# Performance work log

Measured on AMD Instinct MI355X. Metric: run time of the kernel, lower is better.

Reference implementation:

```python
import jax, jax.numpy as jnp
import numpy as np

EPS = 2e-5
N_ROT = 4  # p4 group: rotations by multiples of 90 degrees (exact via rot90)


def _conv2d(x, w, pad):
    # x: [B, Cin, H, W], w: [Cout, Cin, k, k]
    return jax.lax.conv_general_dilated(
        x, w, window_strides=(1, 1), padding=[(pad, pad), (pad, pad)],
        dimension_numbers=('NCHW', 'OIHW', 'NCHW'))


def _conv_rng(x, w):
    # Lifting (Rn -> G) conv. x: [B, I, H, W], w: [O, I, k, k] -> [B, O, 4, H', W']
    O, I, k, _ = w.shape
    wr = jnp.stack([jnp.rot90(w, r, axes=(-2, -1)) for r in range(N_ROT)])  # [4,O,I,k,k]
    y = _conv2d(x, wr.reshape(N_ROT * O, I, k, k), 0)  # [B, 4*O, H', W']
    B, _, H2, W2 = y.shape
    return y.reshape(B, N_ROT, O, H2, W2).transpose(0, 2, 1, 3, 4)


def _conv_gg(x, w, pad=0):
    # Group (G -> G) conv. x: [B, I, 4, H, W], w: [O, I, 4, k, k] -> [B, O, 4, H', W']
    O, I, _, k, _ = w.shape
    ws = []
    for r in range(N_ROT):
        wr = jnp.rot90(w, r, axes=(-2, -1))      # spatial rotation of the kernel
        wr = jnp.roll(wr, r, axis=2)              # cyclic shift of orientation axis
        ws.append(wr.reshape(O, I * N_ROT, k, k))
    wall = jnp.concatenate(ws, 0)                 # [4*O, I*4, k, k]
    B = x.shape[0]
    y = _conv2d(x.reshape(B, I * N_ROT, x.shape[-2], x.shape[-1]), wall, pad)
    H2, W2 = y.shape[-2:]
    return y.reshape(B, N_ROT, O, H2, W2).transpose(0, 2, 1, 3, 4)


def _att_rng(x, aw):
    # fSpatialAttention on Rn input: channel avg+max pooling -> 7x7 conv -> sigmoid gate.
    # x: [B, C, H, W], aw: [1, 2, 7, 7]
    pooled = jnp.concatenate([x.mean(1, keepdims=True), x.max(1, keepdims=True)], axis=1)
    att = jax.nn.sigmoid(_conv2d(pooled, aw, 3))  # [B,1,H,W], SAME padding
    return x * att


def _att_gg(x, aw):
    # fSpatialAttentionGG on G input: channel avg+max pooling -> equivariant 7x7 GG conv -> sigmoid.
    # x: [B, C, 4, H, W], aw: [1, 2, 4, 7, 7]
    pooled = jnp.concatenate([x.mean(1, keepdims=True), x.max(1, keepdims=True)], axis=1)
    att = jax.nn.sigmoid(_conv_gg(pooled, aw, pad=3))  # [B,1,4,H,W]
    return x * att


def _bn(x, g, b):
    # BatchNorm3d over [B, C, 4, H, W]: per-channel stats over (B, 4, H, W)
    m = x.mean((0, 2, 3, 4), keepdims=True)
    v = x.var((0, 2, 3, 4), keepdims=True)
    return (x - m) * jax.lax.rsqrt(v + EPS) * g.reshape(1, -1, 1, 1, 1) + b.reshape(1, -1, 1, 1, 1)


def _pool(x):
    # max_pooling_Rn: 2x2/2 spatial max pool applied independently per orientation
    return jax.lax.reduce_window(x, -jnp.inf, jax.lax.max,
                                 (1, 1, 1, 2, 2), (1, 1, 1, 2, 2), 'VALID')


def setup_inputs() -> dict:
    key = jax.random.key(0)
    ks = jax.random.split(key, 40)
    B, C = 2048, 10
    d = {'x': jax.random.normal(ks[0], (B, 1, 28, 28), jnp.float32)}
    d['c1_w'] = 0.2 * jax.random.normal(ks[1], (C, 1, 3, 3), jnp.float32)
    d['a1_w'] = 0.1 * jax.random.normal(ks[2], (1, 2, 7, 7), jnp.float32)
    j = 3
    for i in range(2, 7):
        d['c%d_w' % i] = 0.1 * jax.random.normal(ks[j], (C, C, 4, 3, 3), jnp.float32); j += 1
        d['a%d_w' % i] = 0.1 * jax.random.normal(ks[j], (1, 2, 4, 7, 7), jnp.float32); j += 1
    d['c7_w'] = 0.1 * jax.random.normal(ks[j], (10, C, 4, 4, 4), jnp.float32); j += 1
    d['a7_w'] = 0.1 * jax.random.normal(ks[j], (1, 2, 4, 7, 7), jnp.float32); j += 1
    for i in range(1, 7):
        d['bn%d_g' % i] = jnp.ones((C,), jnp.float32)
        d['bn%d_b' % i] = jnp.zeros((C,), jnp.float32)
    return d


def reference(x, c1_w, a1_w, c2_w, a2_w, c3_w, a3_w, c4_w, a4_w, c5_w, a5_w,
              c6_w, a6_w, c7_w, a7_w, bn1_g, bn1_b, bn2_g, bn2_b, bn3_g, bn3_b,
              bn4_g, bn4_b, bn5_g, bn5_b, bn6_g, bn6_b):
    # Dropout is treated as identity (eval mode / deterministic reference).
    out = jax.nn.relu(_bn(_conv_rng(_att_rng(x, a1_w), c1_w), bn1_g, bn1_b))      # [B,10,4,26,26]
    out = jax.nn.relu(_bn(_conv_gg(_att_gg(out, a2_w), c2_w), bn2_g, bn2_b))       # [B,10,4,24,24]
    out = _pool(out)                                                                # [B,10,4,12,12]
    out = jax.nn.relu(_bn(_conv_gg(_att_gg(out, a3_w), c3_w), bn3_g, bn3_b))       # 10x10
    out = jax.nn.relu(_bn(_conv_gg(_att_gg(out, a4_w), c4_w), bn4_g, bn4_b))       # 8x8
    out = jax.nn.relu(_bn(_conv_gg(_att_gg(out, a5_w), c5_w), bn5_g, bn5_b))       # 6x6
    out = jax.nn.relu(_bn(_conv_gg(_att_gg(out, a6_w), c6_w), bn6_g, bn6_b))       # 4x4
    out = _conv_gg(_att_gg(out, a7_w), c7_w)                                        # [B,10,4,1,1]
    out = out.max(axis=2)                                                           # group max-pool over orientations
    return out.reshape(out.shape[0], 10)
```

## Files before the change

kernel.cpp:

```cpp
#include <hip/hip_runtime.h>
#include <hip/hip_bf16.h>
#include <cstddef>

typedef __hip_bfloat16 bf;
typedef __attribute__((ext_vector_type(8))) short short8x;
typedef __attribute__((ext_vector_type(4))) float f32x4;

__device__ __forceinline__ float ldv(const float* p){ return *p; }
__device__ __forceinline__ float ldv(const bf* p){ return __bfloat162float(*p); }
__device__ __forceinline__ void stv(float* p, float v){ *p = v; }
__device__ __forceinline__ void stv(bf* p, float v){ *p = __float2bfloat16(v); }
__device__ __forceinline__ float sigm(float x){ return 1.f/(1.f + __expf(-x)); }
__device__ __forceinline__ short bfbits(float v){
  __hip_bfloat16 h = __float2bfloat16(v);
  return *(short*)&h;
}

__device__ __forceinline__ float ldin(const void* p, long i, int f32){
  return f32 ? ((const float*)p)[i] : __bfloat162float(((const bf*)p)[i]);
}

template<int K>
__device__ __forceinline__ int rot_src(int r, int t){
  int u = t / K, v = t % K;
  int s1 = v*K + (K-1-u);
  int s2 = (K-1-u)*K + (K-1-v);
  int s3 = (K-1-v)*K + u;
  return r==0 ? t : (r==1 ? s1 : (r==2 ? s2 : s3));
}

__global__ void k_detect(const void* x, int* ctrl){
  int lane = threadIdx.x;
  float mx = 0.f;
  for (int i = lane; i < 2048; i += 64){
    float v = __bfloat162float(((const bf*)x)[i]);
    if (v != v) v = 1e30f;
    mx = fmaxf(mx, fabsf(v));
  }
  #pragma unroll
  for (int off = 32; off > 0; off >>= 1) mx = fmaxf(mx, __shfl_xor(mx, off));
  if (lane == 0) ctrl[0] = (mx > 1e6f) ? 1 : 0;
}

__global__ __launch_bounds__(256) void k_build_bt(const void* c2, const void* c3, const void* c4,
                                                  const int* __restrict__ ctrl, short* __restrict__ btg){
  const void* ws[3] = {c2, c3, c4};
  const void* cw = ws[blockIdx.x];
  short* outp = btg + blockIdx.x * 18432;
  int f32 = ctrl[0];
  for (int i = threadIdx.x; i < 18432; i += 256){
    int t, n, k;
    bool valid;
    if (i < 13824){
      t = i / 1536;
      int rem = i % 1536;
      int kq = rem / 384;
      n = (i >> 3) % 48;
      k = kq*8 + (i & 7);
      valid = (n < 40);
    } else {
      int j2 = i - 13824;
      int tg = j2 / 1536;
      int lq = (j2 % 1536) / 384;
      n = (j2 >> 3) % 48;
      k = 32 + (i & 7);
      t = tg*4 + lq;
      valid = (t < 9) && (n < 40);
    }
    float v = 0.f;
    if (valid){
      int o = n >> 2, r = n & 3, ci = k >> 2, s = k & 3;
      v = ldin(cw, ((o*10 + ci)*4 + ((s - r) & 3))*9 + rot_src<3>(r, t), f32);
    }
    outp[i] = bfbits(v);
  }
}

__global__ __launch_bounds__(256) void k_l1(const void* __restrict__ x,
                                            const void* __restrict__ a1,
                                            const void* __restrict__ c1,
                                            const int* __restrict__ ctrl,
                                            float* __restrict__ xa,
                                            float* __restrict__ ssum, float* __restrict__ ssq){
  __shared__ float xs[784];
  __shared__ float ws[49];
  __shared__ float xg[28*29];
  __shared__ float wr1[360];
  __shared__ float lsum[16], lss[16];
  int b = blockIdx.x, tid = threadIdx.x;
  int f32 = ctrl[0];
  for (int i = tid; i < 784; i += 256) xs[i] = ldin(x, (long)b*784 + i, f32);
  if (tid < 49) ws[tid] = ldin(a1, tid, f32) + ldin(a1, 49 + tid, f32);
  for (int i = tid; i < 360; i += 256){
    int r = i / 90, rem = i % 90, o = rem / 9, t = rem % 9;
    wr1[i] = ldin(c1, o*9 + rot_src<3>(r, t), f32);
  }
  if (tid < 16){ lsum[tid] = 0.f; lss[tid] = 0.f; }
  __syncthreads();
  for (int p = tid; p < 784; p += 256){
    int h = p / 28, w = p % 28;
    float acc = 0.f;
    #pragma unroll
    for (int u = 0; u < 7; ++u){
      int hh = h + u - 3;
      if (hh < 0 || hh >= 28) continue;
      #pragma unroll
      for (int v = 0; v < 7; ++v){
        int ww = w + v - 3;
        if (ww < 0 || ww >= 28) continue;
        acc = fmaf(xs[hh*28 + ww], ws[u*7 + v], acc);
      }
    }
    float g = xs[p] * sigm(acc);
    xg[h*29 + w] = g;
    xa[(size_t)b*784 + p] = g;
  }
  __syncthreads();
  for (int it = tid; it < 1040; it += 256){
    int o = it / 104, rem = it % 104, r = rem / 26, h = rem % 26;
    float wt[9];
    #pragma unroll
    for (int t = 0; t < 9; ++t) wt[t] = wr1[(r*10 + o)*9 + t];
    float acc[26];
    #pragma unroll
    for (int w = 0; w < 26; ++w) acc[w] = 0.f;
    #pragma unroll
    for (int u = 0; u < 3; ++u){
      float rr[28];
      #pragma unroll
      for (int j = 0; j < 28; ++j) rr[j] = xg[(h + u)*29 + j];
      #pragma unroll
      for (int v = 0; v < 3; ++v){
        float wv = wt[u*3 + v];
        #pragma unroll
        for (int w = 0; w < 26; ++w) acc[w] = fmaf(rr[w + v], wv, acc[w]);
      }
    }
    float s1 = 0.f, s2 = 0.f;
    #pragma unroll
    for (int w = 0; w < 26; ++w){ s1 += acc[w]; s2 += acc[w]*acc[w]; }
    atomicAdd(&lsum[o], s1); atomicAdd(&lss[o], s2);
  }
  __syncthreads();
  if (tid < 10){ atomicAdd(&ssum[tid], lsum[tid]); atomicAdd(&ssq[tid], lss[tid]); }
}

__global__ void k_finalize(const float* __restrict__ ssum, const float* __restrict__ ssq,
                           const void* __restrict__ g, const void* __restrict__ bb,
                           const int* __restrict__ ctrl,
                           float invN, float* __restrict__ scale, float* __restrict__ shift){
  int c = threadIdx.x;
  if (c < 10){
    float m = ssum[c] * invN;
    float v = fmaxf(ssq[c] * invN - m*m, 0.f);
    float sc = ldin(g, c, ctrl[0]) * rsqrtf(v + 2e-5f);
    scale[c] = sc;
    shift[c] = ldin(bb, c, ctrl[0]) - m * sc;
  }
}

__global__ __launch_bounds__(128) void k_att2(const float* __restrict__ xa,
                                              const void* __restrict__ c1,
                                              const float* __restrict__ sc1,
                                              const float* __restrict__ sh1,
                                              const void* __restrict__ aw,
                                              const int* __restrict__ ctrl,
                                              float* __restrict__ attf){
  __shared__ float xs[28*29];
  __shared__ float wr1[360];
  __shared__ float ps[8*26*33];
  __shared__ float wl[1568];
  __shared__ float scs[10], shs[10];
  int b = blockIdx.x, tid = threadIdx.x;
  int f32 = ctrl[0];
  for (int i = tid; i < 784; i += 128){
    int row = i / 28, col = i % 28;
    xs[row*29 + col] = xa[(size_t)b*784 + i];
  }
  for (int i = tid; i < 360; i += 128){
    int r = i / 90, rem = i % 90, o = rem / 9, t = rem % 9;
    wr1[i] = ldin(c1, o*9 + rot_src<3>(r, t), f32);
  }
  for (int i = tid; i < 8*26*33; i += 128) ps[i] = 0.f;
  for (int i = tid; i < 1568; i += 128){
    int r = i / 392, rem = i % 392, i2 = rem / 196, s = (rem % 196)/49, t = rem % 49;
    int sp = (s - r) & 3;
    wl[i] = ldin(aw, (i2*4 + sp)*49 + rot_src<7>(r, t), f32);
  }
  if (tid < 10){ scs[tid] = sc1[tid]; shs[tid] = sh1[tid]; }
  __syncthreads();
  if (tid < 104){
    int s = tid / 26, h = tid % 26;
    float msum[26], mmax[26];
    #pragma unroll
    for (int w = 0; w < 26; ++w){ msum[w] = 0.f; mmax[w] = 0.f; }
    for (int o = 0; o < 10; ++o){
      const float* wb = wr1 + (s*10 + o)*9;
      float acc[26];
      #pragma unroll
      for (int w = 0; w < 26; ++w) acc[w] = 0.f;
      #pragma unroll
      for (int u = 0; u < 3; ++u){
        float rr[28];
        #pragma unroll
        for (int j = 0; j < 28; ++j) rr[j] = xs[(h + u)*29 + j];
        #pragma unroll
        for (int v = 0; v < 3; ++v){
          float wv = wb[u*3 + v];
          #pragma unroll
          for (int w = 0; w < 26; ++w) acc[w] = fmaf(rr[w + v], wv, acc[w]);
        }
      }
      float a_sc = scs[o], a_sh = shs[o];
      #pragma unroll
      for (int w = 0; w < 26; ++w){
        float val = fmaxf(fmaf(acc[w], a_sc, a_sh), 0.f);
        msum[w] += val; mmax[w] = fmaxf(mmax[w], val);
      }
    }
    #pragma unroll
    for (int w = 0; w < 26; ++w){
      ps[s*858 + h*33 + 3 + w] = msum[w] * 0.1f;
      ps[(4 + s)*858 + h*33 + 3 + w] = mmax[w];
    }
  }
  __syncthreads();
  if (tid < 104){
    int r = tid / 26, h = tid % 26;
    float acc[26];
    #pragma unroll
    for (int w = 0; w < 26; ++w) acc[w] = 0.f;
    for (int c = 0; c < 8; ++c){
      const float* wb = wl + r*392 + c*49;
      const float* pb = ps + c*858;
      #pragma unroll
      for (int u = 0; u < 7; ++u){
        int row = h + u - 3;
        if (row < 0 || row >= 26) continue;
        float rr[32];
        #pragma unroll
        for (int j = 0; j < 32; ++j) rr[j] = pb[row*33 + j];
        #pragma unroll
        for (int v = 0; v < 7; ++v){
          float wv = wb[u*7 + v];
          #pragma unroll
          for (int w = 0; w < 26; ++w) acc[w] = fmaf(rr[w + v], wv, acc[w]);
        }
      }
    }
    size_t base = ((size_t)b*4 + r)*676 + (size_t)h*26;
    #pragma unroll
    for (int w = 0; w < 26; ++w) attf[base + w] = sigm(acc[w]);
  }
}

__global__ __launch_bounds__(512, 4) void k_conv2m(const float* __restrict__ xa,
                                                const void* __restrict__ c1,
                                                const float* __restrict__ sc1,
                                                const float* __restrict__ sh1,
                                                const float* __restrict__ attm,
                                                const short* __restrict__ btg,
                                                const int* __restrict__ ctrl,
                                                bf* __restrict__ ap2,
                                                float* __restrict__ ssum, float* __restrict__ ssq){
  __shared__ alignas(16) float xs2[784];
  __shared__ float wr1[360];
  __shared__ alignas(16) float attL[4*676];
  __shared__ alignas(16) short xin[676*40];
  __shared__ float lsum[16], lss[16];
  int tid = threadIdx.x, b = blockIdx.x;
  int f32 = ctrl[0];
  for (int i = tid; i < 784; i += 512) xs2[i] = xa[(size_t)b*784 + i];
  for (int i = tid; i < 360; i += 512){
    int r = i / 90, rem = i % 90, o = rem / 9, t = rem % 9;
    wr1[i] = ldin(c1, o*9 + rot_src<3>(r, t), f32);
  }
  for (int i = tid; i < 2704; i += 512) attL[i] = attm[(size_t)b*2704 + i];
  if (tid < 16){ lsum[tid] = 0.f; lss[tid] = 0.f; }
  __syncthreads();
  for (int it = tid; it < 1040; it += 512){
    int row = it / 40, ch = it % 40;
    int ci = ch >> 2, s = ch & 3;
    float wt[9];
    {
      const float* wb = wr1 + (s*10 + ci)*9;
      #pragma unroll
      for (int t = 0; t < 9; ++t) wt[t] = wb[t];
    }
    float sc = sc1[ci], sh = sh1[ci];
    float acc[26];
    #pragma unroll
    for (int w = 0; w < 26; ++w) acc[w] = 0.f;
    #pragma unroll
    for (int u = 0; u < 3; ++u){
      float rr[28];
      const float4* rp = (const float4*)(xs2 + (row + u)*28);
      #pragma unroll
      for (int j = 0; j < 7; ++j){ float4 q = rp[j]; rr[4*j]=q.x; rr[4*j+1]=q.y; rr[4*j+2]=q.z; rr[4*j+3]=q.w; }
      #pragma unroll
      for (int v = 0; v < 3; ++v){
        float wv = wt[u*3 + v];
        #pragma unroll
        for (int w = 0; w < 26; ++w) acc[w] = fmaf(rr[w + v], wv, acc[w]);
      }
    }
    const float* ap = attL + s*676 + row*26;
    #pragma unroll
    for (int w = 0; w < 26; ++w){
      float v = fmaxf(fmaf(acc[w], sc, sh), 0.f) * ap[w];
      xin[(row*26 + w)*40 + ch] = bfbits(v);
    }
  }
  __syncthreads();

  int wv = tid >> 6, lane = tid & 63, lm = lane & 15, lq = lane >> 4;
  short8x bmain[9], btail[3];
  int tdh[3], tdw[3];
  #pragma unroll
  for (int tg = 0; tg < 3; ++tg){
    int tap = tg*4 + lq; if (tap > 8) tap = 8;
    tdh[tg] = tap / 3; tdw[tg] = tap % 3;
  }
  int curNt = -1, n = 0, o = 0;
  for (int u = wv; u < 54; u += 8){
    int nt = u / 18, mp = u % 18;
    if (nt != curNt){
      curNt = nt; n = nt*16 + lm; o = n >> 2;
      #pragma unroll
      for (int t = 0; t < 9; ++t)
        bmain[t] = *(const short8x*)(btg + (((t*4 + lq)*48 + n) << 3));
      #pragma unroll
      for (int tg = 0; tg < 3; ++tg)
        btail[tg] = *(const short8x*)(btg + 13824 + (((tg*4 + lq)*48 + n) << 3));
    }
    int mt0 = mp*2, mt1 = mp*2 + 1;
    int mA0 = mt0*16 + lm, mA1 = mt1*16 + lm;
    int qi0 = mA0 >> 2, sub0 = mA0 & 3;
    int h00 = 2*(qi0/12) + (sub0 >> 1), w00 = 2*(qi0%12) + (sub0 & 1);
    int qi1 = mA1 >> 2, sub1 = mA1 & 3;
    int h01 = 2*(qi1/12) + (sub1 >> 1), w01 = 2*(qi1%12) + (sub1 & 1);
    f32x4 acc0 = {0.f,0.f,0.f,0.f}, acc1 = {0.f,0.f,0.f,0.f};
    #pragma unroll
    for (int t = 0; t < 9; ++t){
      int sp0 = (h00 + t/3)*26 + (w00 + t%3);
      int sp1 = (h01 + t/3)*26 + (w01 + t%3);
      short8x a0 = *(const short8x*)&xin[sp0*40 + lq*8];
      short8x a1 = *(const short8x*)&xin[sp1*40 + lq*8];
      acc0 = __builtin_amdgcn_mfma_f32_16x16x32_bf16(a0, bmain[t], acc0, 0, 0, 0);
      acc1 = __builtin_amdgcn_mfma_f32_16x16x32_bf16(a1, bmain[t], acc1, 0, 0, 0);
    }
    #pragma unroll
    for (int tg = 0; tg < 3; ++tg){
      int sp0 = (h00 + tdh[tg])*26 + (w00 + tdw[tg]);
      int sp1 = (h01 + tdh[tg])*26 + (w01 + tdw[tg]);
      short8x a0 = *(const short8x*)&xin[sp0*40 + 32];
      short8x a1 = *(const short8x*)&xin[sp1*40 + 32];
      acc0 = __builtin_amdgcn_mfma_f32_16x16x32_bf16(a0, btail[tg], acc0, 0, 0, 0);
      acc1 = __builtin_amdgcn_mfma_f32_16x16x32_bf16(a1, btail[tg], acc1, 0, 0, 0);
    }
    if (n < 40){
      float s1 = acc0[0]+acc0[1]+acc0[2]+acc0[3] + acc1[0]+acc1[1]+acc1[2]+acc1[3];
      float s2 = acc0[0]*acc0[0]+acc0[1]*acc0[1]+acc0[2]*acc0[2]+acc0[3]*acc0[3]
               + acc1[0]*acc1[0]+acc1[1]*acc1[1]+acc1[2]*acc1[2]+acc1[3]*acc1[3];
      atomicAdd(&lsum[o], s1); atomicAdd(&lss[o], s2);
      float mx0 = fmaxf(fmaxf(acc0[0], acc0[1]), fmaxf(acc0[2], acc0[3]));
      float mx1 = fmaxf(fmaxf(acc1[0], acc1[1]), fmaxf(acc1[2], acc1[3]));
      size_t pbase = ((size_t)b*40 + n)*144;
      stv(ap2 + pbase + mt0*4 + lq, mx0);
      stv(ap2 + pbase + mt1*4 + lq, mx1);
    }
  }
  __syncthreads();
  if (tid < 10){ atomicAdd(&ssum[tid], lsum[tid]); atomicAdd(&ssq[tid], lss[tid]); }
}

template<int HIN, int WIN, int NT, typename TI>
__global__ __launch_bounds__(NT) void k_conv_ggm(const TI* __restrict__ act,
                                                 const float* __restrict__ scale,
                                                 const float* __restrict__ shift,
                                                 const float* __restrict__ attm,
                                                 const short* __restrict__ btg,
                                                 float* __restrict__ out,
                                                 float* __restrict__ ssum, float* __restrict__ ssq){
  constexpr int HOUT = HIN - 2, WOUT = WIN - 2;
  constexpr int M = HOUT*WOUT, HW = HIN*WIN;
  constexpr int MT = (M + 15)/16, MU = (MT + 1)/2, UNITS = MU*3;
  constexpr int NWV = NT/64;
  __shared__ alignas(16) short xin[HW*40];
  __shared__ float lsum[16], lss[16];
  int tid = threadIdx.x, b = blockIdx.x;
  if (tid < 16){ lsum[tid] = 0.f; lss[tid] = 0.f; }
  for (int i = tid; i < HW*40; i += NT){
    int sp = i / 40, ch = i % 40;
    int ci = ch >> 2, s = ch & 3;
    float a = ldv(act + ((size_t)b*40 + ch)*HW + sp);
    a = fmaxf(fmaf(a, scale[ci], shift[ci]), 0.f);
    xin[i] = bfbits(a * attm[((size_t)b*4 + s)*HW + sp]);
  }
  __syncthreads();
  int wv = tid >> 6, lane = tid & 63, lm = lane & 15, lq = lane >> 4;
  short8x bmain[9], btail[3];
  int tdh[3], tdw[3];
  #pragma unroll
  for (int tg = 0; tg < 3; ++tg){
    int tap = tg*4 + lq; if (tap > 8) tap = 8;
    tdh[tg] = tap / 3; tdw[tg] = tap % 3;
  }
  int curNt = -1, n = 0, o = 0;
  for (int u = wv; u < UNITS; u += NWV){
    int nt = u / MU, mu = u % MU;
    if (nt != curNt){
      curNt = nt; n = nt*16 + lm; o = n >> 2;
      #pragma unroll
      for (int t = 0; t < 9; ++t)
        bmain[t] = *(const short8x*)(btg + (((t*4 + lq)*48 + n) << 3));
      #pragma unroll
      for (int tg = 0; tg < 3; ++tg)
        btail[tg] = *(const short8x*)(btg + 13824 + (((tg*4 + lq)*48 + n) << 3));
    }
    int mt0 = mu*2, mt1 = mu*2 + 1;
    int mA0 = mt0*16 + lm; if (mA0 > M-1) mA0 = M-1;
    int mA1 = mt1*16 + lm; if (mA1 > M-1) mA1 = M-1;
    int mh0 = mA0 / WOUT, mw0 = mA0 % WOUT;
    int mh1 = mA1 / WOUT, mw1 = mA1 % WOUT;
    f32x4 acc0 = {0.f,0.f,0.f,0.f}, acc1 = {0.f,0.f,0.f,0.f};
    #pragma unroll
    for (int t = 0; t < 9; ++t){
      int sp0 = (mh0 + t/3)*WIN + (mw0 + t%3);
      int sp1 = (mh1 + t/3)*WIN + (mw1 + t%3);
      short8x a0 = *(const short8x*)&xin[sp0*40 + lq*8];
      short8x a1 = *(const short8x*)&xin[sp1*40 + lq*8];
      acc0 = __builtin_amdgcn_mfma_f32_16x16x32_bf16(a0, bmain[t], acc0, 0, 0, 0);
      acc1 = __builtin_amdgcn_mfma_f32_16x16x32_bf16(a1, bmain[t], acc1, 0, 0, 0);
    }
    #pragma unroll
    for (int tg = 0; tg < 3; ++tg){
      int sp0 = (mh0 + tdh[tg])*WIN + (mw0 + tdw[tg]);
      int sp1 = (mh1 + tdh[tg])*WIN + (mw1 + tdw[tg]);
      short8x a0 = *(const short8x*)&xin[sp0*40 + 32];
      short8x a1 = *(const short8x*)&xin[sp1*40 + 32];
      acc0 = __builtin_amdgcn_mfma_f32_16x16x32_bf16(a0, btail[tg], acc0, 0, 0, 0);
      acc1 = __builtin_amdgcn_mfma_f32_16x16x32_bf16(a1, btail[tg], acc1, 0, 0, 0);
    }
    if (n < 40){
      float s1 = 0.f, s2 = 0.f;
      size_t obase = ((size_t)b*40 + n)*M;
      #pragma unroll
      for (int reg = 0; reg < 4; ++reg){
        int m0 = mt0*16 + lq*4 + reg;
        if (m0 < M){ float v = acc0[reg]; s1 += v; s2 += v*v; out[obase + m0] = v; }
        int m1 = mt1*16 + lq*4 + reg;
        if (m1 < M){ float v = acc1[reg]; s1 += v; s2 += v*v; out[obase + m1] = v; }
      }
      atomicAdd(&lsum[o], s1); atomicAdd(&lss[o], s2);
    }
  }
  __syncthreads();
  if (tid < 10){ atomicAdd(&ssum[tid], lsum[tid]); atomicAdd(&ssq[tid], lss[tid]); }
}

template<int H, int W, int NT, typename TA>
__global__ __launch_bounds__(NT) void k_att_gg(const TA* __restrict__ act,
                                               const float* __restrict__ scale,
                                               const float* __restrict__ shift,
                                               const void* __restrict__ aw,
                                               const int* __restrict__ ctrl,
                                               float* __restrict__ att){
  constexpr int WG = (W + 6) | 1;
  constexpr int HW = H*W;
  __shared__ float ps[8*H*WG];
  __shared__ float wl[1568];
  int b = blockIdx.x, tid = threadIdx.x;
  int f32 = ctrl[0];
  for (int i = tid; i < 4*H*WG; i += NT){
    int s = i / (H*WG), rem = i % (H*WG), row = rem / WG, col = rem % WG;
    int cc = col - 3;
    float mn = 0.f, mx = 0.f;
    if (cc >= 0 && cc < W){
      float sum = 0.f; mx = 0.f;
      const TA* ap = act + (size_t)b*40*HW + (size_t)s*HW + row*W + cc;
      #pragma unroll
      for (int c = 0; c < 10; ++c){
        float v = fmaxf(fmaf(ldv(ap + (size_t)c*4*HW), scale[c], shift[c]), 0.f);
        sum += v; mx = fmaxf(mx, v);
      }
      mn = sum * 0.1f;
    }
    ps[s*H*WG + row*WG + col] = mn;
    ps[(4 + s)*H*WG + row*WG + col] = mx;
  }
  for (int i = tid; i < 1568; i += NT){
    int r = i / 392, rem = i % 392, i2 = rem / 196, s = (rem % 196)/49, t = rem % 49;
    int sp = (s - r) & 3;
    wl[i] = ldin(aw, (i2*4 + sp)*49 + rot_src<7>(r, t), f32);
  }
  __syncthreads();
  for (int it = tid; it < 4*H; it += NT){
    int r = it / H, h = it % H;
    float acc[W];
    #pragma unroll
    for (int w = 0; w < W; ++w) acc[w] = 0.f;
    for (int c = 0; c < 8; ++c){
      const float* wb = wl + r*392 + c*49;
      const float* pb = ps + c*H*WG;
      #pragma unroll
      for (int u = 0; u < 7; ++u){
        int row = h + u - 3;
        if (row < 0 || row >= H) continue;
        float rr[W + 6];
        #pragma unroll
        for (int j = 0; j < W + 6; ++j) rr[j] = pb[row*WG + j];
        #pragma unroll
        for (int v = 0; v < 7; ++v){
          float wv = wb[u*7 + v];
          #pragma unroll
          for (int w = 0; w < W; ++w) acc[w] = fmaf(rr[w + v], wv, acc[w]);
        }
      }
    }
    size_t base = ((size_t)b*4 + r)*HW + (size_t)h*W;
    #pragma unroll
    for (int w = 0; w < W; ++w) att[base + w] = sigm(acc[w]);
  }
}

template<int HIN, int WIN, int K, int SR, int NT, bool STATS, typename TI, typename TO>
__global__ __launch_bounds__(NT) void k_conv_gg(const TI* __restrict__ act,
                                                const float* __restrict__ scale,
                                                const float* __restrict__ shift,
                                                const float* __restrict__ attm,
                                                const void* __restrict__ cw,
                                                const int* __restrict__ ctrl,
                                                TO* __restrict__ out,
                                                float* __restrict__ ssum, float* __restrict__ ssq){
  constexpr int HOUT = HIN - K + 1;
  constexpr int WOUT = WIN - K + 1;
  constexpr int NS   = HOUT / SR;
  constexpr int WP   = WIN | 1;
  constexpr int NW   = 10*10*4*K*K;
  __shared__ float xin[40*HIN*WP];
  __shared__ float wl[NW];
  __shared__ float lsum[16], lss[16];
  int tid = threadIdx.x;
  int b = blockIdx.x;
  int f32 = ctrl[0];
  for (int i = tid; i < 40*HIN*WP; i += NT){
    int c = i / (HIN*WP), rem = i % (HIN*WP), rr = rem / WP, col = rem % WP;
    float v = 0.f;
    if (col < WIN){
      int ch = c >> 2, s = c & 3;
      float a = ldv(act + ((size_t)b*40 + c)*HIN*WIN + (size_t)rr*WIN + col);
      a = fmaxf(fmaf(a, scale[ch], shift[ch]), 0.f);
      v = a * attm[((size_t)b*4 + s)*HIN*WIN + (size_t)rr*WIN + col];
    }
    xin[i] = v;
  }
  for (int i = tid; i < NW; i += NT) wl[i] = ldin(cw, i, f32);
  if (STATS && tid < 16){ lsum[tid] = 0.f; lss[tid] = 0.f; }
  __syncthreads();
  for (int it = tid; it < 40*NS; it += NT){
    int o = it / (4*NS), rem = it % (4*NS), r = rem / NS, hs = rem % NS;
    int h0 = hs * SR;
    int perm[K*K];
    #pragma unroll
    for (int t = 0; t < K*K; ++t) perm[t] = rot_src<K>(r, t);
    float acc[SR][WOUT];
    #pragma unroll
    for (int a = 0; a < SR; ++a)
      #pragma unroll
      for (int w = 0; w < WOUT; ++w) acc[a][w] = 0.f;
    for (int ci = 0; ci < 10; ++ci){
      #pragma unroll
      for (int s = 0; s < 4; ++s){
        int sp = (s - r) & 3;
        const float* wb = wl + (size_t)((o*10 + ci)*4 + sp)*K*K;
        float wt[K*K];
        #pragma unroll
        for (int t = 0; t < K*K; ++t) wt[t] = wb[perm[t]];
        const float* ib = xin + (ci*4 + s)*HIN*WP;
        #pragma unroll
        for (int ri = 0; ri < SR + K - 1; ++ri){
          float rr[WP];
          #pragma unroll
          for (int j = 0; j < WP; ++j) rr[j] = ib[(h0 + ri)*WP + j];
          #pragma unroll
          for (int u = 0; u < K; ++u){
            int orr = ri - u;
            if (orr < 0 || orr >= SR) continue;
            #pragma unroll
            for (int v = 0; v < K; ++v){
              float wv = wt[u*K + v];
              #pragma unroll
              for (int w = 0; w < WOUT; ++w) acc[orr][w] = fmaf(rr[w + v], wv, acc[orr][w]);
            }
          }
        }
      }
    }
    if (STATS){
      float s1 = 0.f, s2 = 0.f;
      #pragma unroll
      for (int a = 0; a < SR; ++a)
        #pragma unroll
        for (int w = 0; w < WOUT; ++w){ s1 += acc[a][w]; s2 += acc[a][w]*acc[a][w]; }
      atomicAdd(&lsum[o], s1); atomicAdd(&lss[o], s2);
    }
    #pragma unroll
    for (int a = 0; a < SR; ++a){
      size_t base = ((size_t)b*40 + o*4 + r)*HOUT*WOUT + (size_t)(h0 + a)*WOUT;
      #pragma unroll
      for (int w = 0; w < WOUT; ++w) stv(out + base + w, acc[a][w]);
    }
  }
  if (STATS){
    __syncthreads();
    if (tid < 10){ atomicAdd(&ssum[tid], lsum[tid]); atomicAdd(&ssq[tid], lss[tid]); }
  }
}

__global__ __launch_bounds__(256) void k_out_max(const float* __restrict__ y7, void* __restrict__ outp,
                                                 const int* __restrict__ ctrl){
  int idx = blockIdx.x * 256 + threadIdx.x;
  if (idx >= 20480) return;
  int f32 = ctrl[0];
  const float* p = y7 + (size_t)idx*4;
  float m = fmaxf(fmaxf(p[0], p[1]), fmaxf(p[2], p[3]));
  if (f32) ((float*)outp)[idx] = m;
  else stv((bf*)outp + idx, m);
}

extern "C" void kernel_launch(void* const* d_in, const int* in_sizes, int n_in,
                              void* d_out, int out_size, void* d_ws, size_t ws_size,
                              hipStream_t stream){
  (void)in_sizes; (void)n_in; (void)out_size; (void)ws_size;
  const void* x  = d_in[0];
  const void* c1 = d_in[1];
  const void* a1 = d_in[2];
  const void* c2 = d_in[3];
  const void* a2 = d_in[4];
  const void* c3 = d_in[5];
  const void* a3 = d_in[6];
  const void* c4 = d_in[7];
  const void* a4 = d_in[8];
  const void* c5 = d_in[9];
  const void* a5 = d_in[10];
  const void* c6 = d_in[11];
  const void* a6 = d_in[12];
  const void* c7 = d_in[13];
  const void* a7 = d_in[14];
  const void* bng[6] = {d_in[15],d_in[17],d_in[19],d_in[21],d_in[23],d_in[25]};
  const void* bnb[6] = {d_in[16],d_in[18],d_in[20],d_in[22],d_in[24],d_in[26]};

  size_t off = 0;
  char* wsb = (char*)d_ws;
  auto alloc = [&](size_t bytes)->void*{ void* p = wsb + off; off += (bytes + 255) & ~(size_t)255; return p; };
  int*   ctrl   = (int*)alloc(256);
  float* stats  = (float*)alloc(192*sizeof(float));
  float* scales = (float*)alloc(192*sizeof(float));
  short* btfr   = (short*)alloc(3*18432*2);
  char*  region1 = (char*)alloc(28573696);
  bf*    ap2 = (bf*)alloc((size_t)2048*40*144*2);
  float* yD  = (float*)alloc((size_t)2048*40*100*4);
  float* xa    = (float*)region1;
  float* attf2 = (float*)(region1 + 6422528);
  float* yE    = (float*)region1;
  float* attf3 = (float*)(region1 + 20971520);

  hipMemsetAsync(ctrl, 0, 1024, stream);
  k_detect<<<1, 64, 0, stream>>>(x, ctrl);
  k_build_bt<<<3, 256, 0, stream>>>(c2, c3, c4, ctrl, btfr);

  k_l1<<<2048, 256, 0, stream>>>(x, a1, c1, ctrl, xa, stats + 0, stats + 16);
  k_finalize<<<1, 64, 0, stream>>>(stats + 0, stats + 16, bng[0], bnb[0], ctrl, 1.f/5537792.f, scales + 0, scales + 16);

  k_att2<<<2048, 128, 0, stream>>>(xa, c1, scales + 0, scales + 16, a2, ctrl, attf2);
  k_conv2m<<<2048, 512, 0, stream>>>(xa, c1, scales + 0, scales + 16, attf2, btfr, ctrl, ap2, stats + 32, stats + 48);
  k_finalize<<<1, 64, 0, stream>>>(stats + 32, stats + 48, bng[1], bnb[1], ctrl, 1.f/4718592.f, scales + 32, scales + 48);

  k_att_gg<12,12,64,bf><<<2048, 64, 0, stream>>>(ap2, scales + 32, scales + 48, a3, ctrl, attf3);
  k_conv_ggm<12,12,256,bf><<<2048, 256, 0, stream>>>(ap2, scales + 32, scales + 48,
                                                     attf3, btfr + 18432, yD, stats + 64, stats + 80);
  k_finalize<<<1, 64, 0, stream>>>(stats + 64, stats + 80, bng[2], bnb[2], ctrl, 1.f/819200.f, scales + 64, scales + 80);

  k_att_gg<10,10,64,float><<<2048, 64, 0, stream>>>(yD, scales + 64, scales + 80, a4, ctrl, attf3);
  k_conv_ggm<10,10,128,float><<<2048, 128, 0, stream>>>(yD, scales + 64, scales + 80,
                                                        attf3, btfr + 36864, yE, stats + 96, stats + 112);
  k_finalize<<<1, 64, 0, stream>>>(stats + 96, stats + 112, bng[3], bnb[3], ctrl, 1.f/524288.f, scales + 96, scales + 112);

  k_att_gg<8,8,64,float><<<2048, 64, 0, stream>>>(yE, scales + 96, scales + 112, a5, ctrl, attf3);
  k_conv_gg<8,8,3,2,192,true,float,float><<<2048, 192, 0, stream>>>(yE, scales + 96, scales + 112,
                                                                attf3, c5, ctrl, yD, stats + 128, stats + 144);
  k_finalize<<<1, 64, 0, stream>>>(stats + 128, stats + 144, bng[4], bnb[4], ctrl, 1.f/294912.f, scales + 128, scales + 144);

  k_att_gg<6,6,64,float><<<2048, 64, 0, stream>>>(yD, scales + 128, scales + 144, a6, ctrl, attf3);
  k_conv_gg<6,6,3,2,128,true,float,float><<<2048, 128, 0, stream>>>(yD, scales + 128, scales + 144,
                                                                attf3, c6, ctrl, yE, stats + 160, stats + 176);
  k_finalize<<<1, 64, 0, stream>>>(stats + 160, stats + 176, bng[5], bnb[5], ctrl, 1.f/131072.f, scales + 160, scales + 176);

  k_att_gg<4,4,64,float><<<2048, 64, 0, stream>>>(yE, scales + 160, scales + 176, a7, ctrl, attf3);
  k_conv_gg<4,4,4,1,64,false,float,float><<<2048, 64, 0, stream>>>(yE, scales + 160, scales + 176,
                                                                attf3, c7, ctrl, yD, (float*)nullptr, (float*)nullptr);
  k_out_max<<<80, 256, 0, stream>>>(yD, d_out, ctrl);
}
```

Measured before the change: 954.0 us.

## Fold BN finalize into consumer kernels, swizzle LDS layout, fuse final conv with max

Removes the six single-block k_finalize launches. Each consumer kernel now computes the BatchNorm scale and shift from the raw sums into shared memory. The last group conv and the orientation max are fused into a new k_conv7 kernel, which drops the k_out_max launch and the yD round trip. The bf16 LDS staging buffer for the MFMA convs uses an XOR-style rotation of 8-channel groups by spatial index, meant to reduce bank conflicts on the short8 reads. The cost is that every block recomputes the finalize arithmetic, which is tiny.

```diff
diff --git a/kernel.cpp b/kernel.cpp
--- a/kernel.cpp
+++ b/kernel.cpp
@@ -27,6 +27,18 @@
   int s2 = (K-1-u)*K + (K-1-v);
   int s3 = (K-1-v)*K + u;
   return r==0 ? t : (r==1 ? s1 : (r==2 ? s2 : s3));
+}
+
+__device__ __forceinline__ void finalize10(const float* ssum, const float* ssq,
+                                           const void* g, const void* bb, int f32, float invN,
+                                           float* scs, float* shs, int tid){
+  if (tid < 10){
+    float m = ssum[tid] * invN;
+    float v = fmaxf(ssq[tid] * invN - m*m, 0.f);
+    float sc = ldin(g, tid, f32) * rsqrtf(v + 2e-5f);
+    scs[tid] = sc;
+    shs[tid] = ldin(bb, tid, f32) - m * sc;
+  }
 }
 
 __global__ void k_detect(const void* x, int* ctrl){
@@ -145,24 +157,11 @@
   if (tid < 10){ atomicAdd(&ssum[tid], lsum[tid]); atomicAdd(&ssq[tid], lss[tid]); }
 }
 
-__global__ void k_finalize(const float* __restrict__ ssum, const float* __restrict__ ssq,
-                           const void* __restrict__ g, const void* __restrict__ bb,
-                           const int* __restrict__ ctrl,
-                           float invN, float* __restrict__ scale, float* __restrict__ shift){
-  int c = threadIdx.x;
-  if (c < 10){
-    float m = ssum[c] * invN;
-    float v = fmaxf(ssq[c] * invN - m*m, 0.f);
-    float sc = ldin(g, c, ctrl[0]) * rsqrtf(v + 2e-5f);
-    scale[c] = sc;
-    shift[c] = ldin(bb, c, ctrl[0]) - m * sc;
-  }
-}
-
 __global__ __launch_bounds__(128) void k_att2(const float* __restrict__ xa,
                                               const void* __restrict__ c1,
-                                              const float* __restrict__ sc1,
-                                              const float* __restrict__ sh1,
+                                              const float* __restrict__ pss, const float* __restrict__ psq,
+                                              const void* __restrict__ pg, const void* __restrict__ pb,
+                                              float pinvN,
                                               const void* __restrict__ aw,
                                               const int* __restrict__ ctrl,
                                               float* __restrict__ attf){
@@ -187,7 +186,7 @@
     int sp = (s - r) & 3;
     wl[i] = ldin(aw, (i2*4 + sp)*49 + rot_src<7>(r, t), f32);
   }
-  if (tid < 10){ scs[tid] = sc1[tid]; shs[tid] = sh1[tid]; }
+  finalize10(pss, psq, pg, pb, f32, pinvN, scs, shs, tid);
   __syncthreads();
   if (tid < 104){
     int s = tid / 26, h = tid % 26;
@@ -232,14 +231,14 @@
     for (int w = 0; w < 26; ++w) acc[w] = 0.f;
     for (int c = 0; c < 8; ++c){
       const float* wb = wl + r*392 + c*49;
-      const float* pb = ps + c*858;
+      const float* pb2 = ps + c*858;
       #pragma unroll
       for (int u = 0; u < 7; ++u){
         int row = h + u - 3;
         if (row < 0 || row >= 26) continue;
         float rr[32];
         #pragma unroll
-        for (int j = 0; j < 32; ++j) rr[j] = pb[row*33 + j];
+        for (int j = 0; j < 32; ++j) rr[j] = pb2[row*33 + j];
         #pragma unroll
         for (int v = 0; v < 7; ++v){
           float wv = wb[u*7 + v];
@@ -256,8 +255,9 @@
 
 __global__ __launch_bounds__(512, 4) void k_conv2m(const float* __restrict__ xa,
                                                 const void* __restrict__ c1,
-                                                const float* __restrict__ sc1,
-                                                const float* __restrict__ sh1,
+                                                const float* __restrict__ pss, const float* __restrict__ psq,
+                                                const void* __restrict__ pg, const void* __restrict__ pb,
+                                                float pinvN,
                                                 const float* __restrict__ attm,
                                                 const short* __restrict__ btg,
                                                 const int* __restrict__ ctrl,
@@ -267,6 +267,7 @@
   __shared__ float wr1[360];
   __shared__ alignas(16) float attL[4*676];
   __shared__ alignas(16) short xin[676*40];
+  __shared__ float scs[10], shs[10];
   __shared__ float lsum[16], lss[16];
   int tid = threadIdx.x, b = blockIdx.x;
   int f32 = ctrl[0];
@@ -276,6 +277,7 @@
     wr1[i] = ldin(c1, o*9 + rot_src<3>(r, t), f32);
   }
   for (int i = tid; i < 2704; i += 512) attL[i] = attm[(size_t)b*2704 + i];
+  finalize10(pss, psq, pg, pb, f32, pinvN, scs, shs, tid);
   if (tid < 16){ lsum[tid] = 0.f; lss[tid] = 0.f; }
   __syncthreads();
   for (int it = tid; it < 1040; it += 512){
@@ -287,7 +289,7 @@
       #pragma unroll
       for (int t = 0; t < 9; ++t) wt[t] = wb[t];
     }
-    float sc = sc1[ci], sh = sh1[ci];
+    float sc = scs[ci], sh = shs[ci];
     float acc[26];
     #pragma unroll
     for (int w = 0; w < 26; ++w) acc[w] = 0.f;
@@ -305,10 +307,14 @@
       }
     }
     const float* ap = attL + s*676 + row*26;
+    int chv = ch >> 3, chl = ch & 7;
     #pragma unroll
     for (int w = 0; w < 26; ++w){
       float v = fmaxf(fmaf(acc[w], sc, sh), 0.f) * ap[w];
-      xin[(row*26 + w)*40 + ch] = bfbits(v);
+      int sp = row*26 + w;
+      int phys = (ch < 32) ? sp*40 + (((chv + (sp>>3)) & 3) << 3) + chl
+                           : sp*40 + ch;
+      xin[phys] = bfbits(v);
     }
   }
   __syncthreads();
@@ -344,8 +350,8 @@
     for (int t = 0; t < 9; ++t){
       int sp0 = (h00 + t/3)*26 + (w00 + t%3);
       int sp1 = (h01 + t/3)*26 + (w01 + t%3);
-      short8x a0 = *(const short8x*)&xin[sp0*40 + lq*8];
-      short8x a1 = *(const short8x*)&xin[sp1*40 + lq*8];
+      short8x a0 = *(const short8x*)&xin[sp0*40 + (((lq + (sp0>>3)) & 3) << 3)];
+      short8x a1 = *(const short8x*)&xin[sp1*40 + (((lq + (sp1>>3)) & 3) << 3)];
       acc0 = __builtin_amdgcn_mfma_f32_16x16x32_bf16(a0, bmain[t], acc0, 0, 0, 0);
       acc1 = __builtin_amdgcn_mfma_f32_16x16x32_bf16(a1, bmain[t], acc1, 0, 0, 0);
     }
@@ -376,10 +382,12 @@
 
 template<int HIN, int WIN, int NT, typename TI>
 __global__ __launch_bounds__(NT) void k_conv_ggm(const TI* __restrict__ act,
-                                                 const float* __restrict__ scale,
-                                                 const float* __restrict__ shift,
+                                                 const float* __restrict__ pss, const float* __restrict__ psq,
+                                                 const void* __restrict__ pg, const void* __restrict__ pb,
+                                                 float pinvN,
                                                  const float* __restrict__ attm,
                                                  const short* __restrict__ btg,
+                                                 const int* __restrict__ ctrl,
                                                  float* __restrict__ out,
                                                  float* __restrict__ ssum, float* __restrict__ ssq){
   constexpr int HOUT = HIN - 2, WOUT = WIN - 2;
@@ -387,15 +395,22 @@
   constexpr int MT = (M + 15)/16, MU = (MT + 1)/2, UNITS = MU*3;
   constexpr int NWV = NT/64;
   __shared__ alignas(16) short xin[HW*40];
+  __shared__ float scs[10], shs[10];
   __shared__ float lsum[16], lss[16];
   int tid = threadIdx.x, b = blockIdx.x;
+  int f32 = ctrl[0];
   if (tid < 16){ lsum[tid] = 0.f; lss[tid] = 0.f; }
+  finalize10(pss, psq, pg, pb, f32, pinvN, scs, shs, tid);
+  __syncthreads();
   for (int i = tid; i < HW*40; i += NT){
     int sp = i / 40, ch = i % 40;
     int ci = ch >> 2, s = ch & 3;
     float a = ldv(act + ((size_t)b*40 + ch)*HW + sp);
-    a = fmaxf(fmaf(a, scale[ci], shift[ci]), 0.f);
-    xin[i] = bfbits(a * attm[((size_t)b*4 + s)*HW + sp]);
+    a = fmaxf(fmaf(a, scs[ci], shs[ci]), 0.f);
+    float v = a * attm[((size_t)b*4 + s)*HW + sp];
+    int phys = (ch < 32) ? sp*40 + ((((ch>>3) + (sp>>3)) & 3) << 3) + (ch & 7)
+                         : sp*40 + ch;
+    xin[phys] = bfbits(v);
   }
   __syncthreads();
   int wv = tid >> 6, lane = tid & 63, lm = lane & 15, lq = lane >> 4;
@@ -428,8 +443,8 @@
     for (int t = 0; t < 9; ++t){
       int sp0 = (mh0 + t/3)*WIN + (mw0 + t%3);
       int sp1 = (mh1 + t/3)*WIN + (mw1 + t%3);
-      short8x a0 = *(const short8x*)&xin[sp0*40 + lq*8];
-      short8x a1 = *(const short8x*)&xin[sp1*40 + lq*8];
+      short8x a0 = *(const short8x*)&xin[sp0*40 + (((lq + (sp0>>3)) & 3) << 3)];
+      short8x a1 = *(const short8x*)&xin[sp1*40 + (((lq + (sp1>>3)) & 3) << 3)];
       acc0 = __builtin_amdgcn_mfma_f32_16x16x32_bf16(a0, bmain[t], acc0, 0, 0, 0);
       acc1 = __builtin_amdgcn_mfma_f32_16x16x32_bf16(a1, bmain[t], acc1, 0, 0, 0);
     }
@@ -461,8 +476,9 @@
 
 template<int H, int W, int NT, typename TA>
 __global__ __launch_bounds__(NT) void k_att_gg(const TA* __restrict__ act,
-                                               const float* __restrict__ scale,
-                                               const float* __restrict__ shift,
+                                               const float* __restrict__ pss, const float* __restrict__ psq,
+                                               const void* __restrict__ pg, const void* __restrict__ pb,
+                                               float pinvN,
                                                const void* __restrict__ aw,
                                                const int* __restrict__ ctrl,
                                                float* __restrict__ att){
@@ -470,8 +486,16 @@
   constexpr int HW = H*W;
   __shared__ float ps[8*H*WG];
   __shared__ float wl[1568];
+  __shared__ float scs[10], shs[10];
   int b = blockIdx.x, tid = threadIdx.x;
   int f32 = ctrl[0];
+  finalize10(pss, psq, pg, pb, f32, pinvN, scs, shs, tid);
+  for (int i = tid; i < 1568; i += NT){
+    int r = i / 392, rem = i % 392, i2 = rem / 196, s = (rem % 196)/49, t = rem % 49;
+    int sp = (s - r) & 3;
+    wl[i] = ldin(aw, (i2*4 + sp)*49 + rot_src<7>(r, t), f32);
+  }
+  __syncthreads();
   for (int i = tid; i < 4*H*WG; i += NT){
     int s = i / (H*WG), rem = i % (H*WG), row = rem / WG, col = rem % WG;
     int cc = col - 3;
@@ -481,18 +505,13 @@
       const TA* ap = act + (size_t)b*40*HW + (size_t)s*HW + row*W + cc;
       #pragma unroll
       for (int c = 0; c < 10; ++c){
-        float v = fmaxf(fmaf(ldv(ap + (size_t)c*4*HW), scale[c], shift[c]), 0.f);
+        float v = fmaxf(fmaf(ldv(ap + (size_t)c*4*HW), scs[c], shs[c]), 0.f);
         sum += v; mx = fmaxf(mx, v);
       }
       mn = sum * 0.1f;
     }
     ps[s*H*WG + row*WG + col] = mn;
     ps[(4 + s)*H*WG + row*WG + col] = mx;
-  }
-  for (int i = tid; i < 1568; i += NT){
-    int r = i / 392, rem = i % 392, i2 = rem / 196, s = (rem % 196)/49, t = rem % 49;
-    int sp = (s - r) & 3;
-    wl[i] = ldin(aw, (i2*4 + sp)*49 + rot_src<7>(r, t), f32);
   }
   __syncthreads();
   for (int it = tid; it < 4*H; it += NT){
@@ -502,14 +521,14 @@
     for (int w = 0; w < W; ++w) acc[w] = 0.f;
     for (int c = 0; c < 8; ++c){
       const float* wb = wl + r*392 + c*49;
-      const float* pb = ps + c*H*WG;
+      const float* pb2 = ps + c*H*WG;
       #pragma unroll
       for (int u = 0; u < 7; ++u){
         int row = h + u - 3;
         if (row < 0 || row >= H) continue;
         float rr[W + 6];
         #pragma unroll
-        for (int j = 0; j < W + 6; ++j) rr[j] = pb[row*WG + j];
+        for (int j = 0; j < W + 6; ++j) rr[j] = pb2[row*WG + j];
         #pragma unroll
         for (int v = 0; v < 7; ++v){
           float wv = wb[u*7 + v];
@@ -526,8 +545,9 @@
 
 template<int HIN, int WIN, int K, int SR, int NT, bool STATS, typename TI, typename TO>
 __global__ __launch_bounds__(NT) void k_conv_gg(const TI* __restrict__ act,
-                                                const float* __restrict__ scale,
-                                                const float* __restrict__ shift,
+                                                const float* __restrict__ pss, const float* __restrict__ psq,
+                                                const void* __restrict__ pg, const void* __restrict__ pb,
+                                                float pinvN,
                                                 const float* __restrict__ attm,
                                                 const void* __restrict__ cw,
                                                 const int* __restrict__ ctrl,
@@ -540,23 +560,26 @@
   constexpr int NW   = 10*10*4*K*K;
   __shared__ float xin[40*HIN*WP];
   __shared__ float wl[NW];
+  __shared__ float scs[10], shs[10];
   __shared__ float lsum[16], lss[16];
   int tid = threadIdx.x;
   int b = blockIdx.x;
   int f32 = ctrl[0];
+  for (int i = tid; i < NW; i += NT) wl[i] = ldin(cw, i, f32);
+  finalize10(pss, psq, pg, pb, f32, pinvN, scs, shs, tid);
+  if (STATS && tid < 16){ lsum[tid] = 0.f; lss[tid] = 0.f; }
+  __syncthreads();
   for (int i = tid; i < 40*HIN*WP; i += NT){
     int c = i / (HIN*WP), rem = i % (HIN*WP), rr = rem / WP, col = rem % WP;
     float v = 0.f;
     if (col < WIN){
       int ch = c >> 2, s = c & 3;
       float a = ldv(act + ((size_t)b*40 + c)*HIN*WIN + (size_t)rr*WIN + col);
-      a = fmaxf(fmaf(a, scale[ch], shift[ch]), 0.f);
+      a = fmaxf(fmaf(a, scs[ch], shs[ch]), 0.f);
       v = a * attm[((size_t)b*4 + s)*HIN*WIN + (size_t)rr*WIN + col];
     }
     xin[i] = v;
   }
-  for (int i = tid; i < NW; i += NT) wl[i] = ldin(cw, i, f32);
-  if (STATS && tid < 16){ lsum[tid] = 0.f; lss[tid] = 0.f; }
   __syncthreads();
   for (int it = tid; it < 40*NS; it += NT){
     int o = it / (4*NS), rem = it % (4*NS), r = rem / NS, hs = rem % NS;
@@ -618,15 +641,64 @@
   }
 }
 
-__global__ __launch_bounds__(256) void k_out_max(const float* __restrict__ y7, void* __restrict__ outp,
-                                                 const int* __restrict__ ctrl){
-  int idx = blockIdx.x * 256 + threadIdx.x;
-  if (idx >= 20480) return;
+__global__ __launch_bounds__(64) void k_conv7(const float* __restrict__ act,
+                                              const float* __restrict__ pss, const float* __restrict__ psq,
+                                              const void* __restrict__ pg, const void* __restrict__ pb,
+                                              float pinvN,
+                                              const float* __restrict__ attm,
+                                              const void* __restrict__ cw,
+                                              const int* __restrict__ ctrl,
+                                              void* __restrict__ outp){
+  constexpr int WP = 5;
+  __shared__ float xin[40*4*WP];
+  __shared__ float wl[6400];
+  __shared__ float scs[10], shs[10];
+  __shared__ float ybuf[48];
+  int tid = threadIdx.x, b = blockIdx.x;
   int f32 = ctrl[0];
-  const float* p = y7 + (size_t)idx*4;
-  float m = fmaxf(fmaxf(p[0], p[1]), fmaxf(p[2], p[3]));
-  if (f32) ((float*)outp)[idx] = m;
-  else stv((bf*)outp + idx, m);
+  for (int i = tid; i < 6400; i += 64) wl[i] = ldin(cw, i, f32);
+  finalize10(pss, psq, pg, pb, f32, pinvN, scs, shs, tid);
+  __syncthreads();
+  for (int i = tid; i < 40*4*WP; i += 64){
+    int c = i / (4*WP), rem = i % (4*WP), rr = rem / WP, col = rem % WP;
+    float v = 0.f;
+    if (col < 4){
+      int ch = c >> 2, s = c & 3;
+      float a = ldv(act + ((size_t)b*40 + c)*16 + (size_t)rr*4 + col);
+      a = fmaxf(fmaf(a, scs[ch], shs[ch]), 0.f);
+      v = a * attm[((size_t)b*4 + s)*16 + (size_t)rr*4 + col];
+    }
+    xin[i] = v;
+  }
+  __syncthreads();
+  if (tid < 40){
+    int o = tid >> 2, r = tid & 3;
+    int perm[16];
+    #pragma unroll
+    for (int t = 0; t < 16; ++t) perm[t] = rot_src<4>(r, t);
+    float acc = 0.f;
+    for (int ci = 0; ci < 10; ++ci){
+      #pragma unroll
+      for (int s = 0; s < 4; ++s){
+        int sp = (s - r) & 3;
+        const float* wb = wl + ((o*10 + ci)*4 + sp)*16;
+        const float* ib = xin + (ci*4 + s)*4*WP;
+        #pragma unroll
+        for (int u = 0; u < 4; ++u)
+          #pragma unroll
+          for (int v = 0; v < 4; ++v)
+            acc = fmaf(ib[u*WP + v], wb[perm[u*4 + v]], acc);
+      }
+    }
+    ybuf[tid] = acc;
+  }
+  __syncthreads();
+  if (tid < 10){
+    const float* p = ybuf + tid*4;
+    float m = fmaxf(fmaxf(p[0], p[1]), fmaxf(p[2], p[3]));
+    if (f32) ((float*)outp)[(size_t)b*10 + tid] = m;
+    else stv((bf*)outp + (size_t)b*10 + tid, m);
+  }
 }
 
 extern "C" void kernel_launch(void* const* d_in, const int* in_sizes, int n_in,
@@ -656,7 +728,6 @@
   auto alloc = [&](size_t bytes)->void*{ void* p = wsb + off; off += (bytes + 255) & ~(size_t)255; return p; };
   int*   ctrl   = (int*)alloc(256);
   float* stats  = (float*)alloc(192*sizeof(float));
-  float* scales = (float*)alloc(192*sizeof(float));
   short* btfr   = (short*)alloc(3*18432*2);
   char*  region1 = (char*)alloc(28573696);
   bf*    ap2 = (bf*)alloc((size_t)2048*40*144*2);
@@ -666,39 +737,36 @@
   float* yE    = (float*)region1;
   float* attf3 = (float*)(region1 + 20971520);
 
+  const float iN1 = 1.f/5537792.f, iN2 = 1.f/4718592.f, iN3 = 1.f/819200.f;
+  const float iN4 = 1.f/524288.f, iN5 = 1.f/294912.f, iN6 = 1.f/131072.f;
+
   hipMemsetAsync(ctrl, 0, 1024, stream);
   k_detect<<<1, 64, 0, stream>>>(x, ctrl);
   k_build_bt<<<3, 256, 0, stream>>>(c2, c3, c4, ctrl, btfr);
 
   k_l1<<<2048, 256, 0, stream>>>(x, a1, c1, ctrl, xa, stats + 0, stats + 16);
-  k_finalize<<<1, 64, 0, stream>>>(stats + 0, stats + 16, bng[0], bnb[0], ctrl, 1.f/5537792.f, scales + 0, scales + 16);
-
-  k_att2<<<2048, 128, 0, stream>>>(xa, c1, scales + 0, scales + 16, a2, ctrl, attf2);
-  k_conv2m<<<2048, 512, 0, stream>>>(xa, c1, scales + 0, scales + 16, attf2, btfr, ctrl, ap2, stats + 32, stats + 48);
-  k_finalize<<<1, 64, 0, stream>>>(stats + 32, stats + 48, bng[1], bnb[1], ctrl, 1.f/4718592.f, scales + 32, scales + 48);
-
-  k_att_gg<12,12,64,bf><<<2048, 64, 0, stream>>>(ap2, scales + 32, scales + 48, a3, ctrl, attf3);
-  k_conv_ggm<12,12,256,bf><<<2048, 256, 0, stream>>>(ap2, scales + 32, scales + 48,
-                                                     attf3, btfr + 18432, yD, stats + 64, stats + 80);
-  k_finalize<<<1, 64, 0, stream>>>(stats + 64, stats + 80, bng[2], bnb[2], ctrl, 1.f/819200.f, scales + 64, scales + 80);
-
-  k_att_gg<10,10,64,float><<<2048, 64, 0, stream>>>(yD, scales + 64, scales + 80, a4, ctrl, attf3);
-  k_conv_ggm<10,10,128,float><<<2048, 128, 0, stream>>>(yD, scales + 64, scales + 80,
-                                                        attf3, btfr + 36864, yE, stats + 96, stats + 112);
-  k_finalize<<<1, 64, 0, stream>>>(stats + 96, stats + 112, bng[3], bnb[3], ctrl, 1.f/524288.f, scales + 96, scales + 112);
-
-  k_att_gg<8,8,64,float><<<2048, 64, 0, stream>>>(yE, scales + 96, scales + 112, a5, ctrl, attf3);
-  k_conv_gg<8,8,3,2,192,true,float,float><<<2048, 192, 0, stream>>>(yE, scales + 96, scales + 112,
+
+  k_att2<<<2048, 128, 0, stream>>>(xa, c1, stats + 0, stats + 16, bng[0], bnb[0], iN1, a2, ctrl, attf2);
+  k_conv2m<<<2048, 512, 0, stream>>>(xa, c1, stats + 0, stats + 16, bng[0], bnb[0], iN1,
+                                     attf2, btfr, ctrl, ap2, stats + 32, stats + 48);
+
+  k_att_gg<12,12,64,bf><<<2048, 64, 0, stream>>>(ap2, stats + 32, stats + 48, bng[1], bnb[1], iN2, a3, ctrl, attf3);
+  k_conv_ggm<12,12,256,bf><<<2048, 256, 0, stream>>>(ap2, stats + 32, stats + 48, bng[1], bnb[1], iN2,
+                                                     attf3, btfr + 18432, ctrl, yD, stats + 64, stats + 80);
+
+  k_att_gg<10,10,64,float><<<2048, 64, 0, stream>>>(yD, stats + 64, stats + 80, bng[2], bnb[2], iN3, a4, ctrl, attf3);
+  k_conv_ggm<10,10,128,float><<<2048, 128, 0, stream>>>(yD, stats + 64, stats + 80, bng[2], bnb[2], iN3,
+                                                        attf3, btfr + 36864, ctrl, yE, stats + 96, stats + 112);
+
+  k_att_gg<8,8,64,float><<<2048, 64, 0, stream>>>(yE, stats + 96, stats + 112, bng[3], bnb[3], iN4, a5, ctrl, attf3);
+  k_conv_gg<8,8,3,2,192,true,float,float><<<2048, 192, 0, stream>>>(yE, stats + 96, stats + 112, bng[3], bnb[3], iN4,
                                                                 attf3, c5, ctrl, yD, stats + 128, stats + 144);
-  k_finalize<<<1, 64, 0, stream>>>(stats + 128, stats + 144, bng[4], bnb[4], ctrl, 1.f/294912.f, scales + 128, scales + 144);
-
-  k_att_gg<6,6,64,float><<<2048, 64, 0, stream>>>(yD, scales + 128, scales + 144, a6, ctrl, attf3);
-  k_conv_gg<6,6,3,2,128,true,float,float><<<2048, 128, 0, stream>>>(yD, scales + 128, scales + 144,
+
+  k_att_gg<6,6,64,float><<<2048, 64, 0, stream>>>(yD, stats + 128, stats + 144, bng[4], bnb[4], iN5, a6, ctrl, attf3);
+  k_conv_gg<6,6,3,2,128,true,float,float><<<2048, 128, 0, stream>>>(yD, stats + 128, stats + 144, bng[4], bnb[4], iN5,
                                                                 attf3, c6, ctrl, yE, stats + 160, stats + 176);
-  k_finalize<<<1, 64, 0, stream>>>(stats + 160, stats + 176, bng[5], bnb[5], ctrl, 1.f/131072.f, scales + 160, scales + 176);
-
-  k_att_gg<4,4,64,float><<<2048, 64, 0, stream>>>(yE, scales + 160, scales + 176, a7, ctrl, attf3);
-  k_conv_gg<4,4,4,1,64,false,float,float><<<2048, 64, 0, stream>>>(yE, scales + 160, scales + 176,
-                                                                attf3, c7, ctrl, yD, (float*)nullptr, (float*)nullptr);
-  k_out_max<<<80, 256, 0, stream>>>(yD, d_out, ctrl);
-}
+
+  k_att_gg<4,4,64,float><<<2048, 64, 0, stream>>>(yE, stats + 160, stats + 176, bng[5], bnb[5], iN6, a7, ctrl, attf3);
+  k_conv7<<<2048, 64, 0, stream>>>(yE, stats + 160, stats + 176, bng[5], bnb[5], iN6,
+                                   attf3, c7, ctrl, d_out);
+}
```

Result: no change. 967.5 us (+1.4%).
